# Kernel optimization log

Hardware: AMD Instinct MI355X
Metric: run time of the kernel (lower is better)

The kernel has to match this reference:

```python
import jax, jax.numpy as jnp
import numpy as np

N_NODES = 50000
N_EDGES = 800000
IN_DIM = 128
HEADS = 8
HEAD_DIM = 16


def setup_inputs() -> dict:
    key = jax.random.key(0)
    ks = jax.random.split(key, 9)
    s = 1.0 / np.sqrt(IN_DIM)
    return {
        "h": jax.random.normal(ks[0], (N_NODES, IN_DIM), dtype=jnp.float32),
        "src": jax.random.randint(ks[1], (N_EDGES,), 0, N_NODES, dtype=jnp.int32),
        "dst": jax.random.randint(ks[2], (N_EDGES,), 0, N_NODES, dtype=jnp.int32),
        "WQ": jax.random.normal(ks[3], (IN_DIM, HEADS * HEAD_DIM), dtype=jnp.float32) * s,
        "bQ": jnp.zeros((HEADS * HEAD_DIM,), dtype=jnp.float32),
        "WK": jax.random.normal(ks[4], (IN_DIM, HEADS * HEAD_DIM), dtype=jnp.float32) * s,
        "bK": jnp.zeros((HEADS * HEAD_DIM,), dtype=jnp.float32),
        "WV": jax.random.normal(ks[5], (IN_DIM, HEADS * HEAD_DIM), dtype=jnp.float32) * s,
        "bV": jnp.zeros((HEADS * HEAD_DIM,), dtype=jnp.float32),
    }


def reference(h, src, dst, WQ, bQ, WK, bK, WV, bV):
    N = h.shape[0]
    sqrt_d = jnp.float32(np.sqrt(HEAD_DIM))
    # node projections, viewed as [N, H, D]
    Q = (h @ WQ + bQ).reshape(N, HEADS, HEAD_DIM)
    K = (h @ WK + bK).reshape(N, HEADS, HEAD_DIM)
    V = (h @ WV + bV).reshape(N, HEADS, HEAD_DIM)
    # edge scores: (K_src . Q_dst) per head, scaled exp with clamp [-5, 5]
    score = jnp.sum(K[src] * Q[dst], axis=-1, keepdims=True)  # [E, H, 1]
    score = jnp.exp(jnp.clip(score / sqrt_d, -5.0, 5.0))
    # segment-softmax denominator z and weighted V sum wV, both scattered to dst
    z = jax.ops.segment_sum(score, dst, num_segments=N)            # [N, H, 1]
    wV = jax.ops.segment_sum(V[src] * score, dst, num_segments=N)  # [N, H, D]
    # possible_empty: divide only where z > 0 (wV is 0 there anyway)
    head_out = jnp.where(z > 0, wV / jnp.where(z > 0, z, 1.0), wV)
    return head_out
```

## Files before the change

### kernel.cpp

```cpp
#include <hip/hip_runtime.h>
#include <math.h>

#define DIM 128
#define N_HEADS 8
#define HD 16
#define CAP 96

typedef __attribute__((ext_vector_type(8))) short bf16x8;
typedef __attribute__((ext_vector_type(4))) float f32x4;

__device__ __forceinline__ unsigned bf16pack2(float a, float b) {
    unsigned ua = __builtin_bit_cast(unsigned, a);
    unsigned ub = __builtin_bit_cast(unsigned, b);
    ua = (ua + 0x7FFFu + ((ua >> 16) & 1u)) >> 16;
    ub = (ub + 0x7FFFu + ((ub >> 16) & 1u)) >> 16;
    return ua | (ub << 16);
}
__device__ __forceinline__ float bf16lo(unsigned p) {
    return __builtin_bit_cast(float, p << 16);
}
__device__ __forceinline__ float bf16hi(unsigned p) {
    return __builtin_bit_cast(float, p & 0xFFFF0000u);
}

__global__ __launch_bounds__(256)
void init_kernel(const float* __restrict__ WQ, const float* __restrict__ bQ,
                 const float* __restrict__ WK, const float* __restrict__ bK,
                 const float* __restrict__ WV, const float* __restrict__ bV,
                 unsigned short* __restrict__ WT, float* __restrict__ bias384,
                 int* __restrict__ cnt, int NB, int N)
{
    if ((int)blockIdx.x < NB) {
        int i = blockIdx.x * 256 + threadIdx.x;
        if (i < N) cnt[i] = 0;
    } else {
        int idx = ((int)blockIdx.x - NB) * 256 + threadIdx.x;
        int c = idx >> 7, k = idx & 127;
        const float* W; const float* b; int col = c & 127;
        if (c < 128)      { W = WQ; b = bQ; }
        else if (c < 256) { W = WK; b = bK; }
        else              { W = WV; b = bV; }
        float v = W[k * DIM + col];
        WT[(size_t)c * DIM + k] = (unsigned short)(bf16pack2(v, 0.0f) & 0xFFFFu);
        if (k == 0) bias384[c] = b[col];
    }
}

__global__ __launch_bounds__(256)
void append_qkv_kernel(const int* __restrict__ src, const int* __restrict__ dst,
                       int* __restrict__ cnt, int* __restrict__ srcsF, int E, int QB,
                       const float* __restrict__ h,
                       const unsigned short* __restrict__ WT,
                       const float* __restrict__ bias384,
                       unsigned* __restrict__ Qd, unsigned* __restrict__ KVd,
                       int N)
{
    __shared__ unsigned short hs[64 * 136];

    if ((int)blockIdx.x >= QB) {
        int e = ((int)blockIdx.x - QB) * 256 + threadIdx.x;
        if (e < E) {
            int d    = dst[e];
            int slot = atomicAdd(&cnt[d], 1);
            if (slot < CAP) srcsF[(size_t)d * CAP + slot] = src[e];
        }
        return;
    }

    const int tid = threadIdx.x;
    const int n0  = blockIdx.x * 64;

    #pragma unroll
    for (int i = 0; i < 4; ++i) {
        int lin  = i * 256 + tid;
        int node = lin >> 4;
        int k0   = (lin & 15) * 8;
        int gn   = n0 + node;
        float4 a0, a1;
        if (gn < N) {
            a0 = *(const float4*)(h + (size_t)gn * DIM + k0);
            a1 = *(const float4*)(h + (size_t)gn * DIM + k0 + 4);
        } else {
            a0 = make_float4(0.f, 0.f, 0.f, 0.f);
            a1 = a0;
        }
        uint4 p = make_uint4(bf16pack2(a0.x, a0.y), bf16pack2(a0.z, a0.w),
                             bf16pack2(a1.x, a1.y), bf16pack2(a1.z, a1.w));
        *(uint4*)(hs + node * 136 + k0) = p;
    }
    __syncthreads();

    const int wave   = tid >> 6;
    const int l      = tid & 63;
    const int lane16 = l & 15;
    const int quad   = l >> 4;
    const int wc0    = wave * 96;

    f32x4 acc[6][4];
    #pragma unroll
    for (int ct = 0; ct < 6; ++ct) {
        float4 bv = *(const float4*)(bias384 + wc0 + ct * 16 + quad * 4);
        #pragma unroll
        for (int rt = 0; rt < 4; ++rt)
            acc[ct][rt] = (f32x4){bv.x, bv.y, bv.z, bv.w};
    }

    #pragma unroll
    for (int ks = 0; ks < 4; ++ks) {
        bf16x8 a[6], b[4];
        #pragma unroll
        for (int ct = 0; ct < 6; ++ct)
            a[ct] = *(const bf16x8*)(WT + (size_t)(wc0 + ct * 16 + lane16) * DIM
                                         + ks * 32 + quad * 8);
        #pragma unroll
        for (int rt = 0; rt < 4; ++rt)
            b[rt] = *(const bf16x8*)(hs + (rt * 16 + lane16) * 136 + ks * 32 + quad * 8);
        #pragma unroll
        for (int ct = 0; ct < 6; ++ct)
            #pragma unroll
            for (int rt = 0; rt < 4; ++rt)
                acc[ct][rt] = __builtin_amdgcn_mfma_f32_16x16x32_bf16(
                    a[ct], b[rt], acc[ct][rt], 0, 0, 0);
    }

    #pragma unroll
    for (int ct = 0; ct < 6; ++ct) {
        const int col = wc0 + ct * 16 + quad * 4;
        #pragma unroll
        for (int rt = 0; rt < 4; ++rt) {
            int gn = n0 + rt * 16 + lane16;
            if (gn >= N) continue;
            f32x4 v = acc[ct][rt];
            uint2 pr = make_uint2(bf16pack2(v[0], v[1]), bf16pack2(v[2], v[3]));
            if (col < 128) {
                *(uint2*)(Qd + (size_t)gn * 64 + (col >> 1)) = pr;
            } else if (col < 256) {
                int c = col - 128;
                *(uint2*)(KVd + (size_t)gn * 128 + ((c >> 3) * 8) + ((c & 4) >> 1)) = pr;
            } else {
                int c = col - 256;
                *(uint2*)(KVd + (size_t)gn * 128 + ((c >> 3) * 8) + 4 + ((c & 4) >> 1)) = pr;
            }
        }
    }
}

__device__ __forceinline__ void agg_chunk16(
    const unsigned* __restrict__ KVd, int eg, int deg, int slot, int c,
    const int* raw,
    float q0, float q1, float q2, float q3,
    float q4, float q5, float q6, float q7,
    float acc[8], float& zs)
{
    bool val[4];
    const uint4* p[4];
    #pragma unroll
    for (int j = 0; j < 4; ++j) {
        int ee = eg + j * 4 + slot;
        val[j] = ee < deg;
        int s  = val[j] ? raw[j] : 0;
        p[j]   = (const uint4*)(KVd + (size_t)s * 128 + c * 8);
    }
    uint4 K[4], V[4];
    #pragma unroll
    for (int j = 0; j < 4; ++j) { K[j] = p[j][0]; V[j] = p[j][1]; }

    float d[4];
    #pragma unroll
    for (int j = 0; j < 4; ++j)
        d[j] = bf16lo(K[j].x) * q0 + bf16hi(K[j].x) * q1
             + bf16lo(K[j].y) * q2 + bf16hi(K[j].y) * q3
             + bf16lo(K[j].z) * q4 + bf16hi(K[j].z) * q5
             + bf16lo(K[j].w) * q6 + bf16hi(K[j].w) * q7;
    #pragma unroll
    for (int j = 0; j < 4; ++j) d[j] += __shfl_xor(d[j], 1);

    #pragma unroll
    for (int j = 0; j < 4; ++j) {
        float pc = fminf(fmaxf(d[j] * 0.25f, -5.0f), 5.0f);
        float w  = val[j] ? __expf(pc) : 0.0f;
        zs += w;
        acc[0] += w * bf16lo(V[j].x); acc[1] += w * bf16hi(V[j].x);
        acc[2] += w * bf16lo(V[j].y); acc[3] += w * bf16hi(V[j].y);
        acc[4] += w * bf16lo(V[j].z); acc[5] += w * bf16hi(V[j].z);
        acc[6] += w * bf16lo(V[j].w); acc[7] += w * bf16hi(V[j].w);
    }
}

__global__ __launch_bounds__(256, 4)
void aggregate_kernel(const int* __restrict__ cnt, const int* __restrict__ srcsF,
                      const unsigned* __restrict__ Qd, const unsigned* __restrict__ KVd,
                      float* __restrict__ out, int N)
{
    const int l      = threadIdx.x & 63;
    const int slot   = l >> 4;
    const int c      = l & 15;
    const int stride = gridDim.x * 4;

    int node = blockIdx.x * 4 + (threadIdx.x >> 6);
    if (node >= N) return;

    int   deg = cnt[node];
    uint4 qd  = *(const uint4*)(Qd + (size_t)node * 64 + c * 4);
    int   pb[8];
    {
        const int* b = srcsF + (size_t)node * CAP;
        #pragma unroll
        for (int j = 0; j < 8; ++j)
            pb[j] = b[((j >> 2) << 4) + ((j & 3) << 2) + slot];
    }

    for (;;) {
        const int  nnode   = node + stride;
        const bool hasNext = nnode < N;

        int ndeg = 0; uint4 nqd = make_uint4(0u, 0u, 0u, 0u); int npb[8];
        #pragma unroll
        for (int j = 0; j < 8; ++j) npb[j] = 0;
        if (hasNext) {
            ndeg = cnt[nnode];
            nqd  = *(const uint4*)(Qd + (size_t)nnode * 64 + c * 4);
            const int* b = srcsF + (size_t)nnode * CAP;
            #pragma unroll
            for (int j = 0; j < 8; ++j)
                npb[j] = b[((j >> 2) << 4) + ((j & 3) << 2) + slot];
        }

        int degc = deg > CAP ? CAP : deg;
        const float q0 = bf16lo(qd.x), q1 = bf16hi(qd.x);
        const float q2 = bf16lo(qd.y), q3 = bf16hi(qd.y);
        const float q4 = bf16lo(qd.z), q5 = bf16hi(qd.z);
        const float q6 = bf16lo(qd.w), q7 = bf16hi(qd.w);

        float acc[8] = {0.f, 0.f, 0.f, 0.f, 0.f, 0.f, 0.f, 0.f};
        float zs = 0.f;

        if (degc > 0)
            agg_chunk16(KVd, 0, degc, slot, c, pb,
                        q0, q1, q2, q3, q4, q5, q6, q7, acc, zs);
        if (degc > 16)
            agg_chunk16(KVd, 16, degc, slot, c, pb + 4,
                        q0, q1, q2, q3, q4, q5, q6, q7, acc, zs);
        for (int eg = 32; eg < degc; eg += 16) {
            int raw[4];
            const int* b = srcsF + (size_t)node * CAP;
            #pragma unroll
            for (int j = 0; j < 4; ++j) {
                int ee = eg + j * 4 + slot;
                raw[j] = b[ee < degc ? ee : 0];
            }
            agg_chunk16(KVd, eg, degc, slot, c, raw,
                        q0, q1, q2, q3, q4, q5, q6, q7, acc, zs);
        }

        #pragma unroll
        for (int j = 0; j < 8; ++j) {
            acc[j] += __shfl_xor(acc[j], 16);
            acc[j] += __shfl_xor(acc[j], 32);
        }
        zs += __shfl_xor(zs, 16);
        zs += __shfl_xor(zs, 32);

        if (slot == 0) {
            float inv = (zs > 0.0f) ? (1.0f / zs) : 0.0f;
            *(float4*)(out + (size_t)node * DIM + c * 8) =
                make_float4(acc[0] * inv, acc[1] * inv, acc[2] * inv, acc[3] * inv);
            *(float4*)(out + (size_t)node * DIM + c * 8 + 4) =
                make_float4(acc[4] * inv, acc[5] * inv, acc[6] * inv, acc[7] * inv);
        }

        if (!hasNext) break;
        node = nnode; deg = ndeg; qd = nqd;
        #pragma unroll
        for (int j = 0; j < 8; ++j) pb[j] = npb[j];
    }
}

extern "C" void kernel_launch(void* const* d_in, const int* in_sizes, int n_in,
                              void* d_out, int out_size, void* d_ws, size_t ws_size,
                              hipStream_t stream) {
    const float* h   = (const float*)d_in[0];
    const int*   src = (const int*)  d_in[1];
    const int*   dst = (const int*)  d_in[2];
    const float* WQ  = (const float*)d_in[3];
    const float* bQ  = (const float*)d_in[4];
    const float* WK  = (const float*)d_in[5];
    const float* bK  = (const float*)d_in[6];
    const float* WV  = (const float*)d_in[7];
    const float* bV  = (const float*)d_in[8];
    float* out = (float*)d_out;

    const int N  = in_sizes[0] / DIM;
    const int E  = in_sizes[1];
    const int NB = (N + 255) / 256;
    const int EB = (E + 255) / 256;
    const int QB = (N + 63) / 64;
    const int nConv = (384 * DIM) / 256;

    char* w = (char*)d_ws;
    unsigned*       Qd      = (unsigned*)w;        w += (size_t)N * 64  * sizeof(unsigned);
    unsigned*       KVd     = (unsigned*)w;        w += (size_t)N * 128 * sizeof(unsigned);
    unsigned short* WT      = (unsigned short*)w;  w += (size_t)384 * DIM * sizeof(unsigned short);
    float*          bias384 = (float*)w;           w += 384 * sizeof(float);
    int*            cnt     = (int*)w;             w += (size_t)N * sizeof(int);
    int*            srcsF   = (int*)w;

    init_kernel<<<NB + nConv, 256, 0, stream>>>(WQ, bQ, WK, bK, WV, bV,
                                                WT, bias384, cnt, NB, N);
    append_qkv_kernel<<<QB + EB, 256, 0, stream>>>(src, dst, cnt, srcsF, E, QB,
                                                   h, WT, bias384, Qd, KVd, N);
    aggregate_kernel<<<2048, 256, 0, stream>>>(cnt, srcsF, Qd, KVd, out, N);
}
```

Before: 223.4 us.

## Store adjacency as 16-bit indices and split append from QKV projection

Source indices in the per-destination bucket table are now stored as 16-bit values, and the bucket capacity drops from 96 to 64. This shrinks the adjacency footprint and the bytes read in aggregation. The edge-append work moves out of the fused projection launch into its own kernel, where each thread handles four edges with vector loads. This gives up the overlap between the append and the MFMA projection and adds a launch. The 16-bit indices and smaller cap are only correct while node count stays below 65536 and in-degree below 64.

```diff
diff --git a/kernel.cpp b/kernel.cpp
--- a/kernel.cpp
+++ b/kernel.cpp
@@ -4,7 +4,7 @@
 #define DIM 128
 #define N_HEADS 8
 #define HD 16
-#define CAP 96
+#define CAP 64
 
 typedef __attribute__((ext_vector_type(8))) short bf16x8;
 typedef __attribute__((ext_vector_type(4))) float f32x4;
@@ -47,26 +47,38 @@
 }
 
 __global__ __launch_bounds__(256)
-void append_qkv_kernel(const int* __restrict__ src, const int* __restrict__ dst,
-                       int* __restrict__ cnt, int* __restrict__ srcsF, int E, int QB,
-                       const float* __restrict__ h,
-                       const unsigned short* __restrict__ WT,
-                       const float* __restrict__ bias384,
-                       unsigned* __restrict__ Qd, unsigned* __restrict__ KVd,
-                       int N)
-{
-    __shared__ unsigned short hs[64 * 136];
-
-    if ((int)blockIdx.x >= QB) {
-        int e = ((int)blockIdx.x - QB) * 256 + threadIdx.x;
-        if (e < E) {
+void append_kernel(const int* __restrict__ src, const int* __restrict__ dst,
+                   int* __restrict__ cnt, unsigned short* __restrict__ srcsF, int E)
+{
+    int t = (blockIdx.x * 256 + threadIdx.x) * 4;
+    if (t + 3 < E) {
+        int4 d4 = *(const int4*)(dst + t);
+        int4 s4 = *(const int4*)(src + t);
+        int sl0 = atomicAdd(&cnt[d4.x], 1);
+        int sl1 = atomicAdd(&cnt[d4.y], 1);
+        int sl2 = atomicAdd(&cnt[d4.z], 1);
+        int sl3 = atomicAdd(&cnt[d4.w], 1);
+        if (sl0 < CAP) srcsF[(size_t)d4.x * CAP + sl0] = (unsigned short)s4.x;
+        if (sl1 < CAP) srcsF[(size_t)d4.y * CAP + sl1] = (unsigned short)s4.y;
+        if (sl2 < CAP) srcsF[(size_t)d4.z * CAP + sl2] = (unsigned short)s4.z;
+        if (sl3 < CAP) srcsF[(size_t)d4.w * CAP + sl3] = (unsigned short)s4.w;
+    } else {
+        for (int e = t; e < E; ++e) {
             int d    = dst[e];
             int slot = atomicAdd(&cnt[d], 1);
-            if (slot < CAP) srcsF[(size_t)d * CAP + slot] = src[e];
-        }
-        return;
-    }
-
+            if (slot < CAP) srcsF[(size_t)d * CAP + slot] = (unsigned short)src[e];
+        }
+    }
+}
+
+__global__ __launch_bounds__(256)
+void qkv_mfma_kernel(const float* __restrict__ h,
+                     const unsigned short* __restrict__ WT,
+                     const float* __restrict__ bias384,
+                     unsigned* __restrict__ Qd, unsigned* __restrict__ KVd,
+                     int N)
+{
+    __shared__ unsigned short hs[64 * 136];
     const int tid = threadIdx.x;
     const int n0  = blockIdx.x * 64;
 
@@ -188,7 +200,8 @@
 }
 
 __global__ __launch_bounds__(256, 4)
-void aggregate_kernel(const int* __restrict__ cnt, const int* __restrict__ srcsF,
+void aggregate_kernel(const int* __restrict__ cnt,
+                      const unsigned short* __restrict__ srcsF,
                       const unsigned* __restrict__ Qd, const unsigned* __restrict__ KVd,
                       float* __restrict__ out, int N)
 {
@@ -204,7 +217,7 @@
     uint4 qd  = *(const uint4*)(Qd + (size_t)node * 64 + c * 4);
     int   pb[8];
     {
-        const int* b = srcsF + (size_t)node * CAP;
+        const unsigned short* b = srcsF + (size_t)node * CAP;
         #pragma unroll
         for (int j = 0; j < 8; ++j)
             pb[j] = b[((j >> 2) << 4) + ((j & 3) << 2) + slot];
@@ -220,7 +233,7 @@
         if (hasNext) {
             ndeg = cnt[nnode];
             nqd  = *(const uint4*)(Qd + (size_t)nnode * 64 + c * 4);
-            const int* b = srcsF + (size_t)nnode * CAP;
+            const unsigned short* b = srcsF + (size_t)nnode * CAP;
             #pragma unroll
             for (int j = 0; j < 8; ++j)
                 npb[j] = b[((j >> 2) << 4) + ((j & 3) << 2) + slot];
@@ -243,7 +256,7 @@
                         q0, q1, q2, q3, q4, q5, q6, q7, acc, zs);
         for (int eg = 32; eg < degc; eg += 16) {
             int raw[4];
-            const int* b = srcsF + (size_t)node * CAP;
+            const unsigned short* b = srcsF + (size_t)node * CAP;
             #pragma unroll
             for (int j = 0; j < 4; ++j) {
                 int ee = eg + j * 4 + slot;
@@ -293,7 +306,7 @@
     const int N  = in_sizes[0] / DIM;
     const int E  = in_sizes[1];
     const int NB = (N + 255) / 256;
-    const int EB = (E + 255) / 256;
+    const int EB = (E / 4 + 255) / 256;
     const int QB = (N + 63) / 64;
     const int nConv = (384 * DIM) / 256;
 
@@ -303,11 +316,11 @@
     unsigned short* WT      = (unsigned short*)w;  w += (size_t)384 * DIM * sizeof(unsigned short);
     float*          bias384 = (float*)w;           w += 384 * sizeof(float);
     int*            cnt     = (int*)w;             w += (size_t)N * sizeof(int);
-    int*            srcsF   = (int*)w;
+    unsigned short* srcsF   = (unsigned short*)w;
 
     init_kernel<<<NB + nConv, 256, 0, stream>>>(WQ, bQ, WK, bK, WV, bV,
                                                 WT, bias384, cnt, NB, N);
-    append_qkv_kernel<<<QB + EB, 256, 0, stream>>>(src, dst, cnt, srcsF, E, QB,
-                                                   h, WT, bias384, Qd, KVd, N);
+    append_kernel<<<EB, 256, 0, stream>>>(src, dst, cnt, srcsF, E);
+    qkv_mfma_kernel<<<QB, 256, 0, stream>>>(h, WT, bias384, Qd, KVd, N);
     aggregate_kernel<<<2048, 256, 0, stream>>>(cnt, srcsF, Qd, KVd, out, N);
 }
```

Result: slower. 230.8 us (+3.3%).
